# Kernel tuning notes

Measured on AMD Instinct MI355X. Metric: run time of the kernel, lower is better.

## Reference

```python
import jax, jax.numpy as jnp
import numpy as np

B, L_Q, L_K, H, D = 8, 2048, 2048, 8, 64
FACTOR = 5
U_PART = max(1, min(FACTOR * int(np.ceil(np.log(L_K + 1))), L_K))  # sample_k = 40
U_TOP = max(1, min(FACTOR * int(np.ceil(np.log(L_Q + 1))), L_Q))   # n_top = 40


def setup_inputs() -> dict:
    key = jax.random.key(0)
    kq, kk, kv, ki = jax.random.split(key, 4)
    queries = jax.random.normal(kq, (B, L_Q, H, D), dtype=jnp.float32)
    keys = jax.random.normal(kk, (B, L_K, H, D), dtype=jnp.float32)
    values = jax.random.normal(kv, (B, L_K, H, D), dtype=jnp.float32)
    # random key-sampling indices (GPU randint in the torch module), shared across B,H
    index_sample = jax.random.randint(ki, (L_Q, U_PART), 0, L_K)
    return {"queries": queries, "keys": keys, "values": values,
            "index_sample": index_sample}


def reference(queries, keys, values, index_sample):
    b, l_q, h, d = queries.shape
    l_k = keys.shape[1]
    # [B, L, H, D] -> [B, H, L, D]
    Q = jnp.transpose(queries, (0, 2, 1, 3))
    K = jnp.transpose(keys, (0, 2, 1, 3))
    V = jnp.transpose(values, (0, 2, 1, 3))

    # --- _prob_QK: sparse sampling + sparsity-measure topk query selection ---
    K_sample = K[:, :, index_sample, :]                     # [B,H,L_Q,S,D]
    Q_K_sample = jnp.einsum('bhqe,bhqse->bhqs', Q, K_sample)
    M = Q_K_sample.max(axis=-1) - Q_K_sample.mean(axis=-1)  # [B,H,L_Q]
    _, M_top = jax.lax.top_k(M, U_TOP)                      # [B,H,u] query indices
    Q_reduce = jnp.take_along_axis(Q, M_top[..., None], axis=2)  # [B,H,u,D]
    scores = jnp.einsum('bhue,bhke->bhuk', Q_reduce, K)     # [B,H,u,L_K]
    scores = scores * (1.0 / np.sqrt(d))

    # --- causal mask for selected queries (mask_flag=True) ---
    key_pos = jnp.arange(l_k)
    causal = key_pos[None, None, None, :] > M_top[..., None]  # key > query pos
    scores = jnp.where(causal, -jnp.inf, scores)

    attn = jax.nn.softmax(scores, axis=-1)                  # dropout in eval mode
    attn_out = jnp.einsum('bhuk,bhkd->bhud', attn, V)       # [B,H,u,D]

    # --- initial context (causal => cumulative sum of V) + scatter update ---
    context = jnp.cumsum(V, axis=2)                         # [B,H,L_Q,D]
    b_idx = jnp.arange(b)[:, None, None]
    h_idx = jnp.arange(h)[None, :, None]
    context = context.at[b_idx, h_idx, M_top].set(attn_out)

    return jnp.transpose(context, (0, 2, 1, 3))             # [B,L_Q,H,D]
```

## Files before the change

### kernel.cpp

```cpp
#include <hip/hip_runtime.h>
#include <math.h>

#define Bb 8
#define Hh 8
#define LQ 2048
#define LK 2048
#define Dd 64
#define Uu 40
#define NCH 64
#define CHUNK (LK / NCH)
#define NSPL 16
#define SM_BLOCKS (Bb * (LQ / 8))
#define PART_BLOCKS (Bb * NCH / 2)
#define ATTN_BLOCKS (Bb * Hh * NSPL)
#define SCAN_BLOCKS (Bb * NCH / 2)

typedef float f32x4 __attribute__((ext_vector_type(4)));
typedef short bf16x8 __attribute__((ext_vector_type(8)));

__device__ __forceinline__ short f2bf(float x) {
    unsigned u = __float_as_uint(x);
    unsigned r = u + 0x7fffu + ((u >> 16) & 1u);
    return (short)(r >> 16);
}

__device__ __forceinline__ bf16x8 pack8(float4 a, float4 b) {
    bf16x8 r;
    r[0] = f2bf(a.x); r[1] = f2bf(a.y); r[2] = f2bf(a.z); r[3] = f2bf(a.w);
    r[4] = f2bf(b.x); r[5] = f2bf(b.y); r[6] = f2bf(b.z); r[7] = f2bf(b.w);
    return r;
}

__global__ __launch_bounds__(256) void k_main(
    const float* __restrict__ Qp, const float* __restrict__ Kp,
    const int* __restrict__ idxs, const float* __restrict__ Vp,
    float* __restrict__ M, float* __restrict__ part)
{
    int t = threadIdx.x;

    if (blockIdx.x >= SM_BLOCKS) {
        int bid2 = blockIdx.x - SM_BLOCKS;
        int b = bid2 >> 5;
        int c = (bid2 & 31) * 2 + (t >> 7);
        int h = (t >> 4) & 7, d4 = (t & 15) * 4;

        const float* vb = Vp + ((size_t)(b * LK + c * CHUNK)) * 512 + h * 64 + d4;
        float4 s = make_float4(0.f, 0.f, 0.f, 0.f);
#pragma unroll 4
        for (int l = 0; l < CHUNK; ++l) {
            float4 v = *reinterpret_cast<const float4*>(vb + (size_t)l * 512);
            s.x += v.x; s.y += v.y; s.z += v.z; s.w += v.w;
        }
        int bh = b * 8 + h;
        *reinterpret_cast<float4*>(&part[(size_t)(bh * NCH + c) * Dd + d4]) = s;
        return;
    }

    int b  = blockIdx.x & 7;
    int qt = blockIdx.x >> 3;
    int lane = t & 63, wave = t >> 6;

    __shared__ int sIdx[8 * Uu];
    for (int i = t; i < 8 * Uu; i += 256)
        sIdx[i] = idxs[(qt * 8) * Uu + i];
    __syncthreads();

    const size_t HD = 512;
    const float* Kb = Kp + (size_t)b * LK * HD + lane * 4;

#pragma unroll
    for (int i = 0; i < 2; ++i) {
        int lq = wave * 2 + i;
        int q  = qt * 8 + lq;
        const int* sI = &sIdx[lq * Uu];
#pragma unroll
        for (int ph = 0; ph < 2; ++ph) {
            f32x4 qa = __builtin_nontemporal_load(
                reinterpret_cast<const f32x4*>(
                    Qp + ((size_t)b * LQ + q) * HD + ph * 256) + lane);

            float mx = -INFINITY, sm = 0.f;
#pragma unroll 8
            for (int s = 0; s < Uu; ++s) {
                int kidx = sI[s];
                f32x4 kv = *reinterpret_cast<const f32x4*>(
                    Kb + (size_t)kidx * HD + ph * 256);
                float p = qa[0] * kv[0] + qa[1] * kv[1]
                        + qa[2] * kv[2] + qa[3] * kv[3];
                p += __shfl_xor(p, 1, 64);
                p += __shfl_xor(p, 2, 64);
                p += __shfl_xor(p, 4, 64);
                p += __shfl_xor(p, 8, 64);
                mx = fmaxf(mx, p); sm += p;
            }
            if ((lane & 15) == 0) {
                int h = ph * 4 + (lane >> 4);
                __builtin_nontemporal_store(
                    mx - sm * (1.0f / Uu), &M[((b * 8 + h) << 11) + q]);
            }
        }
    }
}

__global__ __launch_bounds__(256) void k_topk_scan(
    const float* __restrict__ M, int* __restrict__ Mtop,
    const float* __restrict__ Vp, const float* __restrict__ part,
    float* __restrict__ out)
{
    int t = threadIdx.x;

    if (blockIdx.x < Bb * Hh) {
        int bh = blockIdx.x;
        __shared__ float Ml[LQ];
        for (int j = t; j < LQ; j += 256)
            Ml[j] = M[bh * LQ + j];
        __syncthreads();
        if (t >= 64) return;
        int lane = t;

        float lv = -INFINITY; int li = LQ;
        for (int j = 0; j < 32; ++j) {
            int idx = lane + 64 * j;
            float x = Ml[idx];
            if (x > lv) { lv = x; li = idx; }
        }

        int myp = 0;
        for (int u = 0; u < Uu; ++u) {
            float v = lv; int id = li;
#pragma unroll
            for (int off = 32; off > 0; off >>= 1) {
                float ov = __shfl_xor(v, off, 64);
                int   oi = __shfl_xor(id, off, 64);
                if (ov > v || (ov == v && oi < id)) { v = ov; id = oi; }
            }
            if (u == lane) myp = id;
            if ((id & 63) == lane) {
                Ml[id] = -INFINITY;
                lv = -INFINITY; li = LQ;
                for (int j = 0; j < 32; ++j) {
                    int idx = lane + 64 * j;
                    float x = Ml[idx];
                    if (x > lv) { lv = x; li = idx; }
                }
            }
        }

        int rank = 0;
        for (int j = 0; j < Uu; ++j) {
            int pj = __shfl(myp, j, 64);
            rank += (pj < myp && lane < Uu) ? 1 : 0;
        }
        if (lane < Uu) Mtop[bh * Uu + rank] = myp;
        return;
    }

    int bid2 = blockIdx.x - Bb * Hh;
    int b = bid2 >> 5;
    int ch = (bid2 & 31) * 2 + (t >> 7);
    int t2 = t & 127;
    int h = t2 >> 4, d4 = (t2 & 15) * 4;
    int bh = b * 8 + h;

    float4 run = make_float4(0.f, 0.f, 0.f, 0.f);
    for (int cc = 0; cc < ch; ++cc) {
        float4 p4 = *reinterpret_cast<const float4*>(
            &part[(size_t)(bh * NCH + cc) * Dd + d4]);
        run.x += p4.x; run.y += p4.y; run.z += p4.z; run.w += p4.w;
    }

    int l0 = ch * CHUNK;
    const float* vb = Vp + ((size_t)(b * LK + l0)) * 512 + h * 64 + d4;
    float* ob = out + ((size_t)(b * LQ + l0)) * 512 + h * 64 + d4;
#pragma unroll 4
    for (int l = 0; l < CHUNK; ++l) {
        float4 v = *reinterpret_cast<const float4*>(vb + (size_t)l * 512);
        run.x += v.x; run.y += v.y; run.z += v.z; run.w += v.w;
        *reinterpret_cast<float4*>(ob + (size_t)l * 512) = run;
    }
}

__global__ __launch_bounds__(256) void k_attn(
    const float* __restrict__ Qp, const float* __restrict__ Kp,
    const float* __restrict__ Vp, const int* __restrict__ Mtop,
    float* __restrict__ pacc, float* __restrict__ pl)
{
    int t = threadIdx.x;
    int bh = blockIdx.x >> 4;
    int c  = blockIdx.x & (NSPL - 1);
    int b = bh >> 3, h = bh & 7;
    int lane = t & 63, w = t >> 6;
    int col = lane & 15, hi = lane >> 4;

    __shared__ int sP[48];
    __shared__ __align__(16) short sPl[2][48][80];
    __shared__ float sL[4][48];

    if (t < 48) sP[t] = (t < Uu) ? Mtop[bh * Uu + t] : -1;
    __syncthreads();

    const int pmax = sP[Uu - 1];
    const int qmax0 = sP[15], qmax1 = sP[31];

    bf16x8 qf[3][2];
#pragma unroll
    for (int qb = 0; qb < 3; ++qb) {
        int q = qb * 16 + col;
        int row = sP[q];
#pragma unroll
        for (int ks = 0; ks < 2; ++ks) {
            const float* qp = Qp + (((size_t)b * LQ + max(row, 0)) * Hh + h) * Dd
                              + ks * 32 + hi * 8;
            float4 x = *reinterpret_cast<const float4*>(qp);
            float4 y = *reinterpret_cast<const float4*>(qp + 4);
            bf16x8 f = pack8(x, y);
            if (row < 0) f = (bf16x8)(short)0;
            qf[qb][ks] = f;
        }
    }

    f32x4 oacc[3];
    float lsum[3];
#pragma unroll
    for (int qb = 0; qb < 3; ++qb) { oacc[qb] = (f32x4)0.f; lsum[qb] = 0.f; }

#pragma unroll 1
    for (int j = 0; j < LK / 64 / NSPL; ++j) {
        int k0 = (c + NSPL * j) * 64;
        if (k0 > pmax) break;
        int pb = j & 1;
        int qblo = (k0 <= qmax0) ? 0 : ((k0 <= qmax1) ? 1 : 2);

        bf16x8 af[2];
#pragma unroll
        for (int ks = 0; ks < 2; ++ks) {
            const float* kp = Kp + (((size_t)b * LK + k0 + 16 * w + col) * Hh + h) * Dd
                              + ks * 32 + hi * 8;
            float4 x = *reinterpret_cast<const float4*>(kp);
            float4 y = *reinterpret_cast<const float4*>(kp + 4);
            af[ks] = pack8(x, y);
        }

        float vx[2][8];
#pragma unroll
        for (int ks = 0; ks < 2; ++ks) {
            const float* vb = Vp + (((size_t)b * LK + k0 + ks * 32 + hi * 8) * Hh + h) * Dd
                              + 16 * w + col;
#pragma unroll
            for (int jj = 0; jj < 8; ++jj)
                vx[ks][jj] = vb[(size_t)jj * 512];
        }

#pragma unroll
        for (int qb = 0; qb < 3; ++qb) {
            if (qb < qblo) continue;
            f32x4 s = (f32x4)0.f;
            s = __builtin_amdgcn_mfma_f32_16x16x32_bf16(af[0], qf[qb][0], s, 0, 0, 0);
            s = __builtin_amdgcn_mfma_f32_16x16x32_bf16(af[1], qf[qb][1], s, 0, 0, 0);

            int p = sP[qb * 16 + col];
            int kbase = k0 + 16 * w + hi * 4;
            float e0 = (kbase + 0 <= p) ? __expf(s[0] * 0.125f) : 0.f;
            float e1 = (kbase + 1 <= p) ? __expf(s[1] * 0.125f) : 0.f;
            float e2 = (kbase + 2 <= p) ? __expf(s[2] * 0.125f) : 0.f;
            float e3 = (kbase + 3 <= p) ? __expf(s[3] * 0.125f) : 0.f;
            lsum[qb] += (e0 + e1) + (e2 + e3);

            int q = qb * 16 + col;
            int kl = 16 * w + hi * 4;
            unsigned p01 = (unsigned)(unsigned short)f2bf(e0)
                         | ((unsigned)(unsigned short)f2bf(e1) << 16);
            unsigned p23 = (unsigned)(unsigned short)f2bf(e2)
                         | ((unsigned)(unsigned short)f2bf(e3) << 16);
            *reinterpret_cast<unsigned*>(&sPl[pb][q][kl])     = p01;
            *reinterpret_cast<unsigned*>(&sPl[pb][q][kl + 2]) = p23;
        }
        __syncthreads();

#pragma unroll
        for (int ks = 0; ks < 2; ++ks) {
            float4 x = make_float4(vx[ks][0], vx[ks][1], vx[ks][2], vx[ks][3]);
            float4 y = make_float4(vx[ks][4], vx[ks][5], vx[ks][6], vx[ks][7]);
            bf16x8 vf = pack8(x, y);
#pragma unroll
            for (int qb = 0; qb < 3; ++qb) {
                if (qb < qblo) continue;
                bf16x8 pf = *reinterpret_cast<const bf16x8*>(
                    &sPl[pb][qb * 16 + col][ks * 32 + hi * 8]);
                oacc[qb] = __builtin_amdgcn_mfma_f32_16x16x32_bf16(pf, vf, oacc[qb], 0, 0, 0);
            }
        }
    }

#pragma unroll
    for (int qb = 0; qb < 3; ++qb) {
#pragma unroll
        for (int r = 0; r < 4; ++r) {
            int q = qb * 16 + hi * 4 + r;
            if (q < Uu)
                pacc[(((size_t)bh * NSPL + c) * Uu + q) * Dd + 16 * w + col] = oacc[qb][r];
        }
        lsum[qb] += __shfl_xor(lsum[qb], 16, 64);
        lsum[qb] += __shfl_xor(lsum[qb], 32, 64);
        if (lane < 16) sL[w][qb * 16 + lane] = lsum[qb];
    }
    __syncthreads();
    if (t < Uu)
        pl[((size_t)bh * NSPL + c) * Uu + t] =
            sL[0][t] + sL[1][t] + sL[2][t] + sL[3][t];
}

__global__ __launch_bounds__(256) void k_fixup(
    const int* __restrict__ Mtop, const float* __restrict__ pacc,
    const float* __restrict__ pl, float* __restrict__ out)
{
    int gid = blockIdx.x * 4 + (threadIdx.x >> 6);
    int lane = threadIdx.x & 63;
    int bh = gid / Uu, u = gid % Uu;
    int b = bh >> 3, h = bh & 7;
    int p = Mtop[bh * Uu + u];

    float A = 0.f, L = 0.f;
#pragma unroll
    for (int cc = 0; cc < NSPL; ++cc) {
        A += pacc[(((size_t)bh * NSPL + cc) * Uu + u) * Dd + lane];
        L += pl[((size_t)bh * NSPL + cc) * Uu + u];
    }
    out[(((size_t)b * LQ + p) * Hh + h) * Dd + lane] = A / L;
}

extern "C" void kernel_launch(void* const* d_in, const int* in_sizes, int n_in,
                              void* d_out, int out_size, void* d_ws, size_t ws_size,
                              hipStream_t stream) {
    const float* Qp   = (const float*)d_in[0];
    const float* Kp   = (const float*)d_in[1];
    const float* Vp   = (const float*)d_in[2];
    const int*   idxs = (const int*)d_in[3];
    float* out = (float*)d_out;

    char* w = (char*)d_ws;
    float* M    = (float*)(w);
    int*   Mtop = (int*)  (w + 512 * 1024);
    float* part = (float*)(w + 528 * 1024);
    float* pacc = (float*)(w + 1552 * 1024);
    float* pl   = (float*)(w + 12048 * 1024);

    k_main<<<SM_BLOCKS + PART_BLOCKS, 256, 0, stream>>>(Qp, Kp, idxs, Vp, M, part);
    k_topk_scan<<<Bb * Hh + SCAN_BLOCKS, 256, 0, stream>>>(M, Mtop, Vp, part, out);
    k_attn<<<ATTN_BLOCKS, 256, 0, stream>>>(Qp, Kp, Vp, Mtop, pacc, pl);
    k_fixup<<<Bb * Hh * Uu / 4, 256, 0, stream>>>(Mtop, pacc, pl, out);
}
```

Baseline: 140.4 us.

## Process 128-key tiles per attention block with 512 threads

```diff
diff --git a/kernel.cpp b/kernel.cpp
--- a/kernel.cpp
+++ b/kernel.cpp
@@ -9,10 +9,10 @@
 #define Uu 40
 #define NCH 64
 #define CHUNK (LK / NCH)
-#define NSPL 16
+#define NCC 16
 #define SM_BLOCKS (Bb * (LQ / 8))
 #define PART_BLOCKS (Bb * NCH / 2)
-#define ATTN_BLOCKS (Bb * Hh * NSPL)
+#define ATTN_BLOCKS (Bb * Hh * 8)
 #define SCAN_BLOCKS (Bb * NCH / 2)
 
 typedef float f32x4 __attribute__((ext_vector_type(4)));
@@ -180,21 +180,22 @@
     }
 }
 
-__global__ __launch_bounds__(256) void k_attn(
+__global__ __launch_bounds__(512) void k_attn(
     const float* __restrict__ Qp, const float* __restrict__ Kp,
     const float* __restrict__ Vp, const int* __restrict__ Mtop,
     float* __restrict__ pacc, float* __restrict__ pl)
 {
     int t = threadIdx.x;
-    int bh = blockIdx.x >> 4;
-    int c  = blockIdx.x & (NSPL - 1);
+    int bh = blockIdx.x >> 3;
+    int c  = blockIdx.x & 7;
     int b = bh >> 3, h = bh & 7;
     int lane = t & 63, w = t >> 6;
     int col = lane & 15, hi = lane >> 4;
+    int kh = w >> 2, dblk = w & 3;
 
     __shared__ int sP[48];
-    __shared__ __align__(16) short sPl[2][48][80];
-    __shared__ float sL[4][48];
+    __shared__ __align__(16) short sPl[2][48][136];
+    __shared__ float sL[8][48];
 
     if (t < 48) sP[t] = (t < Uu) ? Mtop[bh * Uu + t] : -1;
     __syncthreads();
@@ -225,8 +226,8 @@
     for (int qb = 0; qb < 3; ++qb) { oacc[qb] = (f32x4)0.f; lsum[qb] = 0.f; }
 
 #pragma unroll 1
-    for (int j = 0; j < LK / 64 / NSPL; ++j) {
-        int k0 = (c + NSPL * j) * 64;
+    for (int j = 0; j < 2; ++j) {
+        int k0 = (c + 8 * j) * 128;
         if (k0 > pmax) break;
         int pb = j & 1;
         int qblo = (k0 <= qmax0) ? 0 : ((k0 <= qmax1) ? 1 : 2);
@@ -244,8 +245,8 @@
         float vx[2][8];
 #pragma unroll
         for (int ks = 0; ks < 2; ++ks) {
-            const float* vb = Vp + (((size_t)b * LK + k0 + ks * 32 + hi * 8) * Hh + h) * Dd
-                              + 16 * w + col;
+            const float* vb = Vp + (((size_t)b * LK + k0 + kh * 64 + ks * 32 + hi * 8) * Hh + h) * Dd
+                              + 16 * dblk + col;
 #pragma unroll
             for (int jj = 0; jj < 8; ++jj)
                 vx[ks][jj] = vb[(size_t)jj * 512];
@@ -275,6 +276,16 @@
             *reinterpret_cast<unsigned*>(&sPl[pb][q][kl])     = p01;
             *reinterpret_cast<unsigned*>(&sPl[pb][q][kl + 2]) = p23;
         }
+        if (qblo > 0) {
+#pragma unroll
+            for (int qb = 0; qb < 3; ++qb) {
+                if (qb >= qblo) continue;
+                int q = qb * 16 + col;
+                int kl = 16 * w + hi * 4;
+                *reinterpret_cast<unsigned*>(&sPl[pb][q][kl])     = 0u;
+                *reinterpret_cast<unsigned*>(&sPl[pb][q][kl + 2]) = 0u;
+            }
+        }
         __syncthreads();
 
 #pragma unroll
@@ -286,7 +297,7 @@
             for (int qb = 0; qb < 3; ++qb) {
                 if (qb < qblo) continue;
                 bf16x8 pf = *reinterpret_cast<const bf16x8*>(
-                    &sPl[pb][qb * 16 + col][ks * 32 + hi * 8]);
+                    &sPl[pb][qb * 16 + col][kh * 64 + ks * 32 + hi * 8]);
                 oacc[qb] = __builtin_amdgcn_mfma_f32_16x16x32_bf16(pf, vf, oacc[qb], 0, 0, 0);
             }
         }
@@ -298,16 +309,20 @@
         for (int r = 0; r < 4; ++r) {
             int q = qb * 16 + hi * 4 + r;
             if (q < Uu)
-                pacc[(((size_t)bh * NSPL + c) * Uu + q) * Dd + 16 * w + col] = oacc[qb][r];
+                pacc[(((size_t)bh * NCC + (c * 2 + kh)) * Uu + q) * Dd + 16 * dblk + col]
+                    = oacc[qb][r];
         }
         lsum[qb] += __shfl_xor(lsum[qb], 16, 64);
         lsum[qb] += __shfl_xor(lsum[qb], 32, 64);
         if (lane < 16) sL[w][qb * 16 + lane] = lsum[qb];
     }
     __syncthreads();
-    if (t < Uu)
-        pl[((size_t)bh * NSPL + c) * Uu + t] =
+    if (t < Uu) {
+        pl[((size_t)bh * NCC + c * 2 + 0) * Uu + t] =
             sL[0][t] + sL[1][t] + sL[2][t] + sL[3][t];
+        pl[((size_t)bh * NCC + c * 2 + 1) * Uu + t] =
+            sL[4][t] + sL[5][t] + sL[6][t] + sL[7][t];
+    }
 }
 
 __global__ __launch_bounds__(256) void k_fixup(
@@ -322,9 +337,9 @@
 
     float A = 0.f, L = 0.f;
 #pragma unroll
-    for (int cc = 0; cc < NSPL; ++cc) {
-        A += pacc[(((size_t)bh * NSPL + cc) * Uu + u) * Dd + lane];
-        L += pl[((size_t)bh * NSPL + cc) * Uu + u];
+    for (int cc = 0; cc < NCC; ++cc) {
+        A += pacc[(((size_t)bh * NCC + cc) * Uu + u) * Dd + lane];
+        L += pl[((size_t)bh * NCC + cc) * Uu + u];
     }
     out[(((size_t)b * LQ + p) * Hh + h) * Dd + lane] = A / L;
 }
@@ -347,6 +362,6 @@
 
     k_main<<<SM_BLOCKS + PART_BLOCKS, 256, 0, stream>>>(Qp, Kp, idxs, Vp, M, part);
     k_topk_scan<<<Bb * Hh + SCAN_BLOCKS, 256, 0, stream>>>(M, Mtop, Vp, part, out);
-    k_attn<<<ATTN_BLOCKS, 256, 0, stream>>>(Qp, Kp, Vp, Mtop, pacc, pl);
+    k_attn<<<ATTN_BLOCKS, 512, 0, stream>>>(Qp, Kp, Vp, Mtop, pacc, pl);
     k_fixup<<<Bb * Hh * Uu / 4, 256, 0, stream>>>(Mtop, pacc, pl, out);
 }
```

Result: no change. 140.3 us (-0.1%).
